# Optimization experiments

Hardware: AMD Instinct MI355X
Metric: run time of the kernel (lower is better)

The kernel has to match this reference:

```python
import jax, jax.numpy as jnp
import numpy as np

NUM_NODES = 200000  # num_user + num_item
DIM_E = 64
NUM_EDGES = 600000
EPS = 1e-12
NEG_SLOPE = 0.01  # F.leaky_relu default


def setup_inputs() -> dict:
    key = jax.random.key(0)
    k1, k2, k3 = jax.random.split(key, 3)
    # xavier_normal on [N, D]: std = sqrt(2/(fan_in+fan_out))
    std = float(np.sqrt(2.0 / (NUM_NODES + DIM_E)))
    id_embedding = jax.random.normal(k1, (NUM_NODES, DIM_E), dtype=jnp.float32) * std
    edge_index = jax.random.randint(k2, (2, NUM_EDGES), 0, NUM_NODES, dtype=jnp.int64)
    weight_vector = jax.random.uniform(k3, (2 * NUM_EDGES, 1), dtype=jnp.float32)
    return {"id_embedding": id_embedding, "edge_index": edge_index,
            "weight_vector": weight_vector}


def _l2_normalize(x):
    # F.normalize(x, p=2, dim=1, eps=1e-12)
    n = jnp.sqrt(jnp.sum(x * x, axis=1, keepdims=True))
    return x / jnp.maximum(n, EPS)


def _leaky_relu(x):
    return jnp.where(x >= 0, x, NEG_SLOPE * x)


def reference(id_embedding, edge_index, weight_vector):
    N = id_embedding.shape[0]
    # symmetrize: cat(edge_index, edge_index[[1,0]])
    ei = jnp.concatenate([edge_index, edge_index[::-1]], axis=1)
    src, dst = ei[0], ei[1]  # messages flow src -> dst (PyG source_to_target)
    cnt = jax.ops.segment_sum(jnp.ones((src.shape[0],), jnp.float32), dst,
                              num_segments=N)[:, None]
    denom = jnp.maximum(cnt, 1.0)  # isolated nodes: sum is 0, mean defined as 0

    def conv(x):
        msg = x[src] * weight_vector            # gather + per-edge scale [2E, D]
        agg = jax.ops.segment_sum(msg, dst, num_segments=N)  # scatter-sum [N, D]
        return agg / denom                      # scatter-mean

    x = _l2_normalize(id_embedding)
    x1 = _leaky_relu(conv(x))
    x2 = _leaky_relu(conv(x1))
    return x + x1 + x2
```

## Files before the change

### kernel.cpp

```cpp
#include <hip/hip_runtime.h>
#include <hip/hip_fp16.h>

#define DIM 64
#define NEG_SLOPE 0.01f
#define BKT 256
#define TILEP 4096
#define STILE 2048

typedef unsigned u32;
typedef unsigned long long u64;


__global__ void k_norm_hist(const float* __restrict__ emb,
                            __half* __restrict__ x0h,
                            const int* __restrict__ p,
                            u32* __restrict__ mat,
                            int N, int E, int rb, int B, int nblkE) {
    int t = threadIdx.x;
    if ((int)blockIdx.x < rb) {
        int lane = t & 63;
        int row  = blockIdx.x * 32 + (t >> 6) * 4 + (lane >> 4);
        int l16  = lane & 15;
        if (row >= N) return;
        float4 v = *(const float4*)(emb + (size_t)row * DIM + l16 * 4);
        float s = v.x * v.x + v.y * v.y + v.z * v.z + v.w * v.w;
        #pragma unroll
        for (int m = 1; m < 16; m <<= 1) s += __shfl_xor(s, m, 64);
        float inv = 1.0f / fmaxf(sqrtf(s), 1e-12f);
        union { uint2 u; __half2 h[2]; } pk;
        pk.h[0] = __floats2half2_rn(v.x * inv, v.y * inv);
        pk.h[1] = __floats2half2_rn(v.z * inv, v.w * inv);
        *(uint2*)(x0h + (size_t)row * DIM + l16 * 4) = pk.u;
    } else {
        __shared__ u32 hist[800];
        int blk = blockIdx.x - rb;
        for (int i = t; i < B; i += 512) hist[i] = 0;
        __syncthreads();
        int base = blk * TILEP;
        #pragma unroll
        for (int k = 0; k < TILEP / 512; k++) {
            int pe = base + k * 512 + t;
            if (pe < E) {
                int a = p[pe];
                int b = p[pe + E];
                atomicAdd(&hist[(u32)b >> 8], 1u);
                atomicAdd(&hist[(u32)a >> 8], 1u);
            }
        }
        __syncthreads();
        for (int i = t; i < B; i += 512) mat[(size_t)i * nblkE + blk] = hist[i];
    }
}

__global__ void k_scan1(const u32* __restrict__ in, u32* __restrict__ out,
                        u32* __restrict__ bsum, int M) {
    __shared__ u32 sdata[256];
    int t = threadIdx.x;
    int base = blockIdx.x * STILE + t * 8;
    u32 v[8]; u32 tsum = 0;
    #pragma unroll
    for (int k = 0; k < 8; k++) {
        int i = base + k;
        v[k] = (i < M) ? in[i] : 0u;
        tsum += v[k];
    }
    sdata[t] = tsum;
    __syncthreads();
    for (int off = 1; off < 256; off <<= 1) {
        u32 x = (t >= off) ? sdata[t - off] : 0u;
        __syncthreads();
        sdata[t] += x;
        __syncthreads();
    }
    u32 run = sdata[t] - tsum;
    if (t == 255) bsum[blockIdx.x] = sdata[255];
    #pragma unroll
    for (int k = 0; k < 8; k++) {
        int i = base + k;
        if (i < M) out[i] = run;
        run += v[k];
    }
}

__global__ void k_scanfix(u32* __restrict__ mscan,
                          const u32* __restrict__ bsum, int nb, int M) {
    __shared__ u32 sdata[256];
    __shared__ u32 sexcl[256];
    int t = threadIdx.x;
    u32 v = (t < nb) ? bsum[t] : 0u;
    sdata[t] = v;
    __syncthreads();
    for (int off = 1; off < 256; off <<= 1) {
        u32 x = (t >= off) ? sdata[t - off] : 0u;
        __syncthreads();
        sdata[t] += x;
        __syncthreads();
    }
    sexcl[t] = sdata[t] - v;
    __syncthreads();
    int i = blockIdx.x * 256 + t;
    if (i < M) mscan[i] += sexcl[i >> 11];
}

__global__ void k_place(const int* __restrict__ p, const float* __restrict__ w,
                        const u32* __restrict__ mscan,
                        u32* __restrict__ pay, unsigned char* __restrict__ loc8,
                        int E, int nblkE, int B) {
    __shared__ u32 cur[800];
    int blk = blockIdx.x;
    int t = threadIdx.x;
    for (int i = t; i < B; i += 512) cur[i] = 0;
    __syncthreads();
    int base = blk * TILEP;
    #pragma unroll
    for (int k = 0; k < TILEP / 512; k++) {
        int pe = base + k * 512 + t;
        if (pe >= E) continue;
        int a = p[pe];
        int b = p[pe + E];
        float wf = w[pe];
        float wb = w[pe + E];
        u32 wf14 = (u32)(wf * 16384.0f + 0.5f); if (wf14 > 16383u) wf14 = 16383u;
        u32 wb14 = (u32)(wb * 16384.0f + 0.5f); if (wb14 > 16383u) wb14 = 16383u;
        u32 bin = (u32)b >> 8;
        u32 rank = atomicAdd(&cur[bin], 1u);
        u32 slot = mscan[(size_t)bin * nblkE + blk] + rank;
        pay[slot]  = ((u32)a << 14) | wf14;
        loc8[slot] = (unsigned char)((u32)b & (BKT - 1));
        u32 bin2 = (u32)a >> 8;
        u32 rank2 = atomicAdd(&cur[bin2], 1u);
        u32 slot2 = mscan[(size_t)bin2 * nblkE + blk] + rank2;
        pay[slot2]  = ((u32)b << 14) | wb14;
        loc8[slot2] = (unsigned char)((u32)a & (BKT - 1));
    }
}

__global__ void k_bucket(const u32* __restrict__ pay,
                         const unsigned char* __restrict__ loc8,
                         const u32* __restrict__ mscan,
                         u32* __restrict__ row_ptr,
                         u32* __restrict__ colw,
                         int N, int E, int B, int nblkE) {
    __shared__ u32 hist[BKT];
    __shared__ u32 excl[BKT];
    __shared__ u32 sdata[256];
    int b = blockIdx.x;
    int t = threadIdx.x;
    int node0 = b * BKT;
    int nnodes = N - node0; if (nnodes > BKT) nnodes = BKT;
    size_t flat0 = (size_t)b * nblkE;
    u32 seg_s = mscan[flat0];
    u32 seg_e = (b + 1 < B) ? mscan[flat0 + nblkE] : (u32)(2 * E);
    hist[t] = 0;
    __syncthreads();
    for (u32 j = seg_s + t; j < seg_e; j += 256)
        atomicAdd(&hist[loc8[j]], 1u);
    __syncthreads();
    u32 tsum = hist[t];
    sdata[t] = tsum;
    __syncthreads();
    for (int off = 1; off < 256; off <<= 1) {
        u32 x = (t >= off) ? sdata[t - off] : 0u;
        __syncthreads();
        sdata[t] += x;
        __syncthreads();
    }
    u32 texcl = sdata[t] - tsum;
    excl[t] = texcl;
    if (t < nnodes) row_ptr[node0 + t] = seg_s + texcl;
    if (b == 0 && t == 0) row_ptr[N] = (u32)(2 * E);
    __syncthreads();
    for (u32 j = seg_s + t; j < seg_e; j += 256) {
        u32 loc = loc8[j];
        u32 pos = atomicAdd(&excl[loc], 1u);
        colw[seg_s + pos] = pay[j];
    }
}


__device__ __forceinline__ void gather8(const __half* __restrict__ x,
                                        const u32* __restrict__ colw,
                                        u32 s, u32 e, int g, int sub,
                                        float acc[8]) {
    for (u32 base = s; base < e; base += 8) {
        int m = (int)(e - base); if (m > 8) m = 8;
        u32 u = 0;
        if (sub < m) u = colw[base + sub];
        int   cx = (int)(u >> 14);
        float cy = (float)(u & 16383u) * (1.0f / 16384.0f);
        for (int j = 0; j < m; j++) {
            int   sj = __shfl(cx, (g << 3) | j, 64);
            float wj = __shfl(cy, (g << 3) | j, 64);
            uint4 q = *(const uint4*)(x + (size_t)sj * DIM + sub * 8);
            const __half2* hp = (const __half2*)&q;
            #pragma unroll
            for (int k = 0; k < 4; k++) {
                float2 f = __half22float2(hp[k]);
                acc[2 * k]     += f.x * wj;
                acc[2 * k + 1] += f.y * wj;
            }
        }
    }
}

__global__ void k_conv1(const __half* __restrict__ x0h,
                        const u32* __restrict__ row_ptr,
                        const u32* __restrict__ colw,
                        __half* __restrict__ x1h, int N) {
    int wave = (blockIdx.x * 256 + threadIdx.x) >> 6;
    int g    = (threadIdx.x >> 3) & 7;
    int sub  = threadIdx.x & 7;
    int row  = wave * 8 + g;
    if (row >= N) return;
    u32 s = row_ptr[row], e = row_ptr[row + 1];
    float acc[8] = {0, 0, 0, 0, 0, 0, 0, 0};
    gather8(x0h, colw, s, e, g, sub, acc);
    float rdeno = 1.0f / fmaxf((float)(e - s), 1.0f);
    __half2 hv[4];
    #pragma unroll
    for (int k = 0; k < 4; k++) {
        float v0 = acc[2 * k] * rdeno;
        float v1 = acc[2 * k + 1] * rdeno;
        v0 = (v0 >= 0.0f) ? v0 : NEG_SLOPE * v0;
        v1 = (v1 >= 0.0f) ? v1 : NEG_SLOPE * v1;
        hv[k] = __floats2half2_rn(v0, v1);
    }
    *(uint4*)(x1h + (size_t)row * DIM + sub * 8) = *(const uint4*)hv;
}

__global__ void k_conv2(const __half* __restrict__ x0h,
                        const __half* __restrict__ x1h,
                        const u32* __restrict__ row_ptr,
                        const u32* __restrict__ colw,
                        float* __restrict__ out, int N) {
    int wave = (blockIdx.x * 256 + threadIdx.x) >> 6;
    int g    = (threadIdx.x >> 3) & 7;
    int sub  = threadIdx.x & 7;
    int row  = wave * 8 + g;
    if (row >= N) return;
    u32 s = row_ptr[row], e = row_ptr[row + 1];
    float acc[8] = {0, 0, 0, 0, 0, 0, 0, 0};
    gather8(x1h, colw, s, e, g, sub, acc);
    float rdeno = 1.0f / fmaxf((float)(e - s), 1.0f);
    uint4 q0 = *(const uint4*)(x0h + (size_t)row * DIM + sub * 8);
    uint4 q1 = *(const uint4*)(x1h + (size_t)row * DIM + sub * 8);
    const __half2* h0 = (const __half2*)&q0;
    const __half2* h1 = (const __half2*)&q1;
    float r[8];
    #pragma unroll
    for (int k = 0; k < 4; k++) {
        float2 a = __half22float2(h0[k]);
        float2 b = __half22float2(h1[k]);
        float x2a = acc[2 * k] * rdeno;
        float x2b = acc[2 * k + 1] * rdeno;
        x2a = (x2a >= 0.0f) ? x2a : NEG_SLOPE * x2a;
        x2b = (x2b >= 0.0f) ? x2b : NEG_SLOPE * x2b;
        r[2 * k]     = a.x + b.x + x2a;
        r[2 * k + 1] = a.y + b.y + x2b;
    }
    float* op = out + (size_t)row * DIM + sub * 8;
    *(float4*)(op)     = make_float4(r[0], r[1], r[2], r[3]);
    *(float4*)(op + 4) = make_float4(r[4], r[5], r[6], r[7]);
}

static inline size_t align16(size_t x) { return (x + 15) & ~(size_t)15; }

extern "C" void kernel_launch(void* const* d_in, const int* in_sizes, int n_in,
                              void* d_out, int out_size, void* d_ws, size_t ws_size,
                              hipStream_t stream) {
    const int N = in_sizes[0] / DIM;
    const int E = in_sizes[1] / 2;

    const float* emb = (const float*)d_in[0];
    const int*   ei  = (const int*)d_in[1];
    const float* w   = (const float*)d_in[2];
    float*       out = (float*)d_out;

    const int B     = (N + BKT - 1) / BKT;
    const int nblkE = (E + TILEP - 1) / TILEP;
    const int M     = B * nblkE;
    const int nb1   = (M + STILE - 1) / STILE;
    const int rb    = (N + 31) / 32;
    const int cvb   = (N + 31) / 32;

    char* ws = (char*)d_ws;
    size_t off = 0;
    __half*        x0h    = (__half*)(ws + off);        off += align16((size_t)N * DIM * 2);
    __half*        x1h    = (__half*)(ws + off);        off += align16((size_t)N * DIM * 2);
    u32*           pay    = (u32*)(ws + off);           off += align16((size_t)2 * E * 4);
    unsigned char* loc8   = (unsigned char*)(ws + off); off += align16((size_t)2 * E);
    u32*           colw   = (u32*)(ws + off);           off += align16((size_t)2 * E * 4);
    u32*           mat    = (u32*)(ws + off);           off += align16((size_t)M * 4);
    u32*           mscan  = (u32*)(ws + off);           off += align16((size_t)M * 4);
    u32*           row_ptr= (u32*)(ws + off);           off += align16((size_t)(N + 1) * 4);
    u32*           bsum   = (u32*)(ws + off);           off += align16(256 * 4);

    k_norm_hist<<<rb + nblkE, 512, 0, stream>>>(emb, x0h, ei, mat, N, E, rb, B, nblkE);
    k_scan1  <<<nb1, 256, 0, stream>>>(mat, mscan, bsum, M);
    k_scanfix<<<(M + 255) / 256, 256, 0, stream>>>(mscan, bsum, nb1, M);
    k_place  <<<nblkE, 512, 0, stream>>>(ei, w, mscan, pay, loc8, E, nblkE, B);
    k_bucket <<<B, 256, 0, stream>>>(pay, loc8, mscan, row_ptr, colw, N, E, B, nblkE);

    k_conv1<<<cvb, 256, 0, stream>>>(x0h, row_ptr, colw, x1h, N);
    k_conv2<<<cvb, 256, 0, stream>>>(x0h, x1h, row_ptr, colw, out, N);
}
```

Measured before the change: 244.2 us.

## Locally sort edge records in shared memory before scattering to buckets

```diff
diff --git a/kernel.cpp b/kernel.cpp
--- a/kernel.cpp
+++ b/kernel.cpp
@@ -5,10 +5,12 @@
 #define NEG_SLOPE 0.01f
 #define BKT 256
 #define TILEP 4096
+#define RECS (TILEP * 2)
 #define STILE 2048
 
 typedef unsigned u32;
-typedef unsigned long long u64;
+typedef unsigned short u16;
+typedef unsigned char u8;
 
 
 __global__ void k_norm_hist(const float* __restrict__ emb,
@@ -102,41 +104,96 @@
     if (i < M) mscan[i] += sexcl[i >> 11];
 }
 
-__global__ void k_place(const int* __restrict__ p, const float* __restrict__ w,
-                        const u32* __restrict__ mscan,
-                        u32* __restrict__ pay, unsigned char* __restrict__ loc8,
-                        int E, int nblkE, int B) {
-    __shared__ u32 cur[800];
+__global__ __launch_bounds__(512, 1)
+void k_place(const int* __restrict__ p, const float* __restrict__ w,
+             const u32* __restrict__ mscan,
+             u32* __restrict__ pay, u8* __restrict__ loc8,
+             int E, int nblkE, int B) {
+    __shared__ u32 sPay[RECS];
+    __shared__ u32 sMeta[RECS];
+    __shared__ u16 sPerm[RECS];
+    __shared__ u32 hist[1024];
+    __shared__ u32 sstart[1024];
+    __shared__ u32 delta[1024];
+    __shared__ u32 sdata[512];
+
     int blk = blockIdx.x;
     int t = threadIdx.x;
-    for (int i = t; i < B; i += 512) cur[i] = 0;
-    __syncthreads();
     int base = blk * TILEP;
+    int rem = E - base;
+    int vlim = rem * 2; if (vlim > RECS) vlim = RECS;
+
+    hist[t] = 0; hist[t + 512] = 0;
+    __syncthreads();
+
     #pragma unroll
     for (int k = 0; k < TILEP / 512; k++) {
         int pe = base + k * 512 + t;
-        if (pe >= E) continue;
-        int a = p[pe];
-        int b = p[pe + E];
-        float wf = w[pe];
-        float wb = w[pe + E];
-        u32 wf14 = (u32)(wf * 16384.0f + 0.5f); if (wf14 > 16383u) wf14 = 16383u;
-        u32 wb14 = (u32)(wb * 16384.0f + 0.5f); if (wb14 > 16383u) wb14 = 16383u;
-        u32 bin = (u32)b >> 8;
-        u32 rank = atomicAdd(&cur[bin], 1u);
-        u32 slot = mscan[(size_t)bin * nblkE + blk] + rank;
-        pay[slot]  = ((u32)a << 14) | wf14;
-        loc8[slot] = (unsigned char)((u32)b & (BKT - 1));
-        u32 bin2 = (u32)a >> 8;
-        u32 rank2 = atomicAdd(&cur[bin2], 1u);
-        u32 slot2 = mscan[(size_t)bin2 * nblkE + blk] + rank2;
-        pay[slot2]  = ((u32)b << 14) | wb14;
-        loc8[slot2] = (unsigned char)((u32)a & (BKT - 1));
+        if (pe < E) {
+            int a = p[pe];
+            int b = p[pe + E];
+            float wf = w[pe];
+            float wb = w[pe + E];
+            u32 wf14 = (u32)(wf * 16384.0f + 0.5f); if (wf14 > 16383u) wf14 = 16383u;
+            u32 wb14 = (u32)(wb * 16384.0f + 0.5f); if (wb14 > 16383u) wb14 = 16383u;
+            int li = (k * 512 + t) * 2;
+            sPay[li]      = ((u32)a << 14) | wf14;
+            sMeta[li]     = (u32)b;
+            sPay[li + 1]  = ((u32)b << 14) | wb14;
+            sMeta[li + 1] = (u32)a;
+            atomicAdd(&hist[(u32)b >> 8], 1u);
+            atomicAdd(&hist[(u32)a >> 8], 1u);
+        }
+    }
+    __syncthreads();
+
+    u32 a0 = hist[2 * t], a1 = hist[2 * t + 1];
+    u32 tsum = a0 + a1;
+    sdata[t] = tsum;
+    __syncthreads();
+    for (int off = 1; off < 512; off <<= 1) {
+        u32 x = (t >= off) ? sdata[t - off] : 0u;
+        __syncthreads();
+        sdata[t] += x;
+        __syncthreads();
+    }
+    u32 texcl = sdata[t] - tsum;
+    sstart[2 * t]     = texcl;
+    sstart[2 * t + 1] = texcl + a0;
+    __syncthreads();
+
+    hist[t] = 0; hist[t + 512] = 0;
+    for (int i = t; i < B; i += 512)
+        delta[i] = mscan[(size_t)i * nblkE + blk] - sstart[i];
+    __syncthreads();
+
+    #pragma unroll
+    for (int k = 0; k < RECS / 512; k++) {
+        int li = k * 512 + t;
+        if (li < vlim) {
+            u32 bin = sMeta[li] >> 8;
+            u32 r = atomicAdd(&hist[bin], 1u);
+            sPerm[sstart[bin] + r] = (u16)li;
+        }
+    }
+    __syncthreads();
+
+    #pragma unroll
+    for (int k = 0; k < RECS / 512; k++) {
+        int j = k * 512 + t;
+        if (j < vlim) {
+            int li = sPerm[j];
+            u32 pv = sPay[li];
+            u32 mt = sMeta[li];
+            u32 gs = (u32)j + delta[mt >> 8];
+            pay[gs]  = pv;
+            loc8[gs] = (u8)(mt & 255u);
+        }
     }
 }
 
 __global__ void k_bucket(const u32* __restrict__ pay,
-                         const unsigned char* __restrict__ loc8,
+                         const u8* __restrict__ loc8,
                          const u32* __restrict__ mscan,
                          u32* __restrict__ row_ptr,
                          u32* __restrict__ colw,
@@ -285,15 +342,15 @@
 
     char* ws = (char*)d_ws;
     size_t off = 0;
-    __half*        x0h    = (__half*)(ws + off);        off += align16((size_t)N * DIM * 2);
-    __half*        x1h    = (__half*)(ws + off);        off += align16((size_t)N * DIM * 2);
-    u32*           pay    = (u32*)(ws + off);           off += align16((size_t)2 * E * 4);
-    unsigned char* loc8   = (unsigned char*)(ws + off); off += align16((size_t)2 * E);
-    u32*           colw   = (u32*)(ws + off);           off += align16((size_t)2 * E * 4);
-    u32*           mat    = (u32*)(ws + off);           off += align16((size_t)M * 4);
-    u32*           mscan  = (u32*)(ws + off);           off += align16((size_t)M * 4);
-    u32*           row_ptr= (u32*)(ws + off);           off += align16((size_t)(N + 1) * 4);
-    u32*           bsum   = (u32*)(ws + off);           off += align16(256 * 4);
+    __half* x0h    = (__half*)(ws + off); off += align16((size_t)N * DIM * 2);
+    __half* x1h    = (__half*)(ws + off); off += align16((size_t)N * DIM * 2);
+    u32*    pay    = (u32*)(ws + off);    off += align16((size_t)2 * E * 4);
+    u8*     loc8   = (u8*)(ws + off);     off += align16((size_t)2 * E);
+    u32*    colw   = (u32*)(ws + off);    off += align16((size_t)2 * E * 4);
+    u32*    mat    = (u32*)(ws + off);    off += align16((size_t)M * 4);
+    u32*    mscan  = (u32*)(ws + off);    off += align16((size_t)M * 4);
+    u32*    row_ptr= (u32*)(ws + off);    off += align16((size_t)(N + 1) * 4);
+    u32*    bsum   = (u32*)(ws + off);    off += align16(256 * 4);
 
     k_norm_hist<<<rb + nblkE, 512, 0, stream>>>(emb, x0h, ei, mat, N, E, rb, B, nblkE);
     k_scan1  <<<nb1, 256, 0, stream>>>(mat, mscan, bsum, M);
```

Result: faster. 210.7 us (-13.7%).
